# Performance work log

Measured on AMD Instinct MI355X. Metric: run time of the kernel, lower is better.

## Reference

```python
import math
import jax, jax.numpy as jnp
import numpy as np

C_Z = 128
C_HID = 128
B, N = 1, 512


def setup_inputs() -> dict:
    key = jax.random.key(0)
    ks = jax.random.split(key, 8)
    s_in = 1.0 / math.sqrt(C_Z)
    s_hid = 1.0 / math.sqrt(C_HID)
    return {
        "z": jax.random.normal(ks[0], (B, N, N, C_Z), dtype=jnp.float32),
        "residue_mask": jnp.ones((B, N), dtype=jnp.bool_),
        "ln_w": jnp.ones((C_Z,), dtype=jnp.float32),
        "ln_b": jnp.zeros((C_Z,), dtype=jnp.float32),
        "a_w": jax.random.uniform(ks[1], (C_Z, C_HID), jnp.float32, -s_in, s_in),
        "a_b": jax.random.uniform(ks[2], (C_HID,), jnp.float32, -s_in, s_in),
        "b_w": jax.random.uniform(ks[3], (C_Z, C_HID), jnp.float32, -s_in, s_in),
        "b_b": jax.random.uniform(ks[4], (C_HID,), jnp.float32, -s_in, s_in),
        "out_w": jax.random.uniform(ks[5], (C_HID, C_Z), jnp.float32, -s_hid, s_hid),
        "out_b": jax.random.uniform(ks[6], (C_Z,), jnp.float32, -s_hid, s_hid),
    }


def _layernorm(x, w, b, eps=1e-5):
    mu = jnp.mean(x, axis=-1, keepdims=True)
    var = jnp.mean(jnp.square(x - mu), axis=-1, keepdims=True)
    return (x - mu) * jax.lax.rsqrt(var + eps) * w + b


def reference(z, residue_mask, ln_w, ln_b, a_w, a_b, b_w, b_b, out_w, out_b):
    # z: [B, N, N, c_z]
    x = _layernorm(z, ln_w, ln_b)
    a = x @ a_w + a_b  # [B, N, N, c_hid]
    b = x @ b_w + b_b  # [B, N, N, c_hid]
    # outgoing: contract over k -> c_hid independent NxN matmuls
    u = jnp.einsum('bikc,bjkc->bijc', a, b)
    u = (u / math.sqrt(max(z.shape[1], 1))) @ out_w + out_b  # [B, N, N, c_z]
    pair = residue_mask[:, :, None] & residue_mask[:, None, :]  # [B, N, N]
    return u * pair[..., None].astype(u.dtype)
```

## Files before the change

kernel.cpp:

```cpp
#include <hip/hip_runtime.h>

#define NRES 512
#define NN   (NRES * NRES)
#define CZ   128

typedef __attribute__((ext_vector_type(8))) short bf16x8;
typedef __attribute__((ext_vector_type(4))) short s16x4;
typedef __attribute__((ext_vector_type(4))) float f32x4;

static __device__ __forceinline__ short f2bf(float f) {
  union { float f; unsigned u; } v; v.f = f;
  unsigned r = v.u + 0x7fffu + ((v.u >> 16) & 1u);
  return (short)(r >> 16);
}

static __device__ __forceinline__ void gload_lds16(const void* g, void* l) {
  __builtin_amdgcn_global_load_lds(
      (__attribute__((address_space(1))) const void*)g,
      (__attribute__((address_space(3))) void*)l, 16, 0, 0);
}

__global__ __launch_bounds__(256) void k_prep(const float* __restrict__ a_w,
                                              const float* __restrict__ b_w,
                                              const float* __restrict__ out_w,
                                              short* __restrict__ w_cat_t,
                                              short* __restrict__ w_out_t) {
  int idx = blockIdx.x * 256 + threadIdx.x;
  if (idx < 256 * 128) {
    int cc = idx >> 7, zz = idx & 127;
    float v = (cc < 128) ? a_w[zz * 128 + cc] : b_w[zz * 128 + (cc - 128)];
    w_cat_t[idx] = f2bf(v);
  } else if (idx < 256 * 128 + 128 * 128) {
    int i2 = idx - 256 * 128;
    int zz = i2 >> 7, cc = i2 & 127;
    w_out_t[i2] = f2bf(out_w[cc * 128 + zz]);
  }
}

__global__ __launch_bounds__(512, 4) void k_lnproj(const float* __restrict__ z,
                                                   const float* __restrict__ ln_w,
                                                   const float* __restrict__ ln_b,
                                                   const float* __restrict__ a_bias,
                                                   const float* __restrict__ b_bias,
                                                   const short* __restrict__ w_cat_t,
                                                   short* __restrict__ a_t,
                                                   short* __restrict__ b_t) {
  __shared__ short xb[64][136];

  const int tid = threadIdx.x;
  const int bid = (int)blockIdx.x;
  const int sb = ((bid & 7) << 9) | (bid >> 3);
  const int r0 = sb * 64;
  const int row = tid >> 3, seg = tid & 7;

  const float4* zg = (const float4*)(z + (size_t)r0 * CZ);
  float4 v[4];
#pragma unroll
  for (int it = 0; it < 4; ++it) v[it] = zg[row * 32 + seg + it * 8];

  float s = 0.f, s2 = 0.f;
#pragma unroll
  for (int it = 0; it < 4; ++it) {
    s  += v[it].x + v[it].y + v[it].z + v[it].w;
    s2 += v[it].x * v[it].x + v[it].y * v[it].y + v[it].z * v[it].z + v[it].w * v[it].w;
  }
  s  += __shfl_xor(s, 1);  s  += __shfl_xor(s, 2);  s  += __shfl_xor(s, 4);
  s2 += __shfl_xor(s2, 1); s2 += __shfl_xor(s2, 2); s2 += __shfl_xor(s2, 4);
  const float mu = s * (1.f / CZ);
  const float rstd = rsqrtf(s2 * (1.f / CZ) - mu * mu + 1e-5f);

  const float4* lw4 = (const float4*)ln_w;
  const float4* lb4 = (const float4*)ln_b;
#pragma unroll
  for (int it = 0; it < 4; ++it) {
    float4 wv = lw4[seg + it * 8], bv = lb4[seg + it * 8];
    s16x4 pk;
    pk[0] = f2bf((v[it].x - mu) * rstd * wv.x + bv.x);
    pk[1] = f2bf((v[it].y - mu) * rstd * wv.y + bv.y);
    pk[2] = f2bf((v[it].z - mu) * rstd * wv.z + bv.z);
    pk[3] = f2bf((v[it].w - mu) * rstd * wv.w + bv.w);
    *(s16x4*)&xb[row][seg * 4 + it * 32] = pk;
  }
  __syncthreads();

  const int w = tid >> 6, l = tid & 63;
  const int q = l >> 4, n16 = l & 15;
  const f32x4 zf = {0.f, 0.f, 0.f, 0.f};
  f32x4 acc[4][2];
#pragma unroll
  for (int a = 0; a < 4; ++a)
#pragma unroll
    for (int b = 0; b < 2; ++b) acc[a][b] = zf;

#pragma unroll
  for (int kk = 0; kk < 4; ++kk) {
    bf16x8 af[4], bfv[2];
#pragma unroll
    for (int rt = 0; rt < 4; ++rt)
      af[rt] = *(const bf16x8*)&xb[rt * 16 + n16][kk * 32 + q * 8];
#pragma unroll
    for (int ct = 0; ct < 2; ++ct) {
      int col = w * 32 + ct * 16 + n16;
      bfv[ct] = *(const bf16x8*)&w_cat_t[col * 128 + kk * 32 + q * 8];
    }
#pragma unroll
    for (int rt = 0; rt < 4; ++rt)
#pragma unroll
      for (int ct = 0; ct < 2; ++ct)
        acc[rt][ct] = __builtin_amdgcn_mfma_f32_16x16x32_bf16(af[rt], bfv[ct], acc[rt][ct], 0, 0, 0);
  }

  __syncthreads();
  short* tb = &xb[0][0] + w * (16 * 66);
#pragma unroll
  for (int ct = 0; ct < 2; ++ct) {
    const int col = w * 32 + ct * 16 + n16;
    const int ch = col & 127;
    const float bias = (col < 128) ? a_bias[ch] : b_bias[ch];
#pragma unroll
    for (int rt = 0; rt < 4; ++rt) {
      s16x4 pk;
#pragma unroll
      for (int rg = 0; rg < 4; ++rg) pk[rg] = f2bf(acc[rt][ct][rg] + bias);
      *(s16x4*)&tb[n16 * 66 + rt * 16 + q * 4] = pk;
    }
#pragma unroll
    for (int i = 0; i < 2; ++i) {
      int ch_l = i * 8 + (l >> 3);
      int rseg = l & 7;
      bf16x8 t = *(const bf16x8*)&tb[ch_l * 66 + rseg * 8];
      int colg = w * 32 + ct * 16 + ch_l;
      *(bf16x8*)&a_t[(size_t)colg * NN + r0 + rseg * 8] = t;
    }
  }
}

__global__ __launch_bounds__(256, 3) void k_einsum(const short* __restrict__ a_t,
                                                   const short* __restrict__ b_t,
                                                   short* __restrict__ u_bf) {
  __shared__ short smem[128 * 134];
  short* As = smem;
  short* Bs = smem + 128 * 64;

  const int bid = blockIdx.x;
  const int xcd = bid & 7;
  const int g = bid >> 3;
  const int c = (xcd << 4) | (g >> 4);
  const int t = g & 15;
  const int ti = t >> 2, tj = t & 3;

  const short* Ab = a_t + (size_t)c * NN + (size_t)(ti * 128) * NRES;
  const short* Bb = b_t + (size_t)c * NN + (size_t)(tj * 128) * NRES;

  const int tid = threadIdx.x, w = tid >> 6, l = tid & 63;
  const int q = l >> 4, n16 = l & 15;
  const int wr = w >> 1, wc = w & 1;

  const int srow = l >> 3;
  const int schk = l & 7;
  const int gchk = schk ^ srow;

  const f32x4 zf = {0.f, 0.f, 0.f, 0.f};
  f32x4 acc[4][4];
#pragma unroll
  for (int a = 0; a < 4; ++a)
#pragma unroll
    for (int b = 0; b < 4; ++b) acc[a][b] = zf;

  for (int st = 0; st < 8; ++st) {
    const int k0 = st * 64;
    __syncthreads();
#pragma unroll
    for (int i = 0; i < 4; ++i) {
      int r = w * 32 + i * 8 + srow;
      gload_lds16(Ab + (size_t)r * NRES + k0 + gchk * 8, &As[(w * 32 + i * 8) * 64 + l * 8]);
      gload_lds16(Bb + (size_t)r * NRES + k0 + gchk * 8, &Bs[(w * 32 + i * 8) * 64 + l * 8]);
    }
    __syncthreads();

#pragma unroll
    for (int kk = 0; kk < 2; ++kk) {
      bf16x8 af[4], bfv[4];
#pragma unroll
      for (int it = 0; it < 4; ++it) {
        int m = wr * 64 + it * 16 + n16;
        af[it] = *(const bf16x8*)&As[m * 64 + ((kk * 4 + q) ^ (m & 7)) * 8];
      }
#pragma unroll
      for (int jt = 0; jt < 4; ++jt) {
        int n = wc * 64 + jt * 16 + n16;
        bfv[jt] = *(const bf16x8*)&Bs[n * 64 + ((kk * 4 + q) ^ (n & 7)) * 8];
      }
#pragma unroll
      for (int jt = 0; jt < 4; ++jt)
#pragma unroll
        for (int it = 0; it < 4; ++it)
          acc[jt][it] = __builtin_amdgcn_mfma_f32_16x16x32_bf16(bfv[jt], af[it], acc[jt][it], 0, 0, 0);
    }
  }

  __syncthreads();
  const float sc = 0.04419417382415922f;
#pragma unroll
  for (int jt = 0; jt < 4; ++jt)
#pragma unroll
    for (int it = 0; it < 4; ++it) {
      s16x4 pk;
#pragma unroll
      for (int rg = 0; rg < 4; ++rg) pk[rg] = f2bf(acc[jt][it][rg] * sc);
      int il = wr * 64 + it * 16 + n16;
      int jl = wc * 64 + jt * 16 + q * 4;
      *(s16x4*)&smem[il * 134 + jl] = pk;
    }
  __syncthreads();

  short* ub = u_bf + (size_t)c * NN + (size_t)(ti * 128) * NRES + tj * 128;
#pragma unroll
  for (int vv = 0; vv < 8; ++vv) {
    int CH = vv * 256 + tid;
    int i = CH >> 4, js = CH & 15;
    bf16x8 tv = *(const bf16x8*)&smem[i * 134 + js * 8];
    *(bf16x8*)&ub[(size_t)i * NRES + js * 8] = tv;
  }
}

#define US_S 130
__global__ __launch_bounds__(256, 3) void k_outproj(const short* __restrict__ u_bf,
                                                    const short* __restrict__ w_out_t,
                                                    const float* __restrict__ out_b,
                                                    const int* __restrict__ mask,
                                                    float* __restrict__ out) {
  __shared__ short Us[128 * US_S];

  const int bid = (int)blockIdx.x;
  const int sb = ((bid & 7) << 8) | (bid >> 3);
  const int m0 = sb * 128;
  const int tid = threadIdx.x, w = tid >> 6, l = tid & 63;
  const int q = l >> 4, n16 = l & 15;
  const int wz = w >> 1, wm = w & 1;

  {
    const int mseg = tid & 15;
    const int cb = tid >> 4;
#pragma unroll
    for (int it = 0; it < 8; ++it) {
      int cc = it * 16 + cb;
      bf16x8 vv = *(const bf16x8*)(u_bf + (size_t)cc * NN + m0 + mseg * 8);
      int base = cc * US_S + mseg * 8;
#pragma unroll
      for (int wi = 0; wi < 4; ++wi) {
        int pk = ((int)(unsigned short)vv[2 * wi + 1] << 16) | (unsigned short)vv[2 * wi];
        *(int*)&Us[base + 2 * wi] = pk;
      }
    }
  }
  __syncthreads();

  const f32x4 zf = {0.f, 0.f, 0.f, 0.f};
  f32x4 acc[4][4];
#pragma unroll
  for (int a = 0; a < 4; ++a)
#pragma unroll
    for (int b = 0; b < 4; ++b) acc[a][b] = zf;

#pragma unroll
  for (int kk = 0; kk < 4; ++kk) {
    bf16x8 af[4];
#pragma unroll
    for (int rt = 0; rt < 4; ++rt) {
      int zz = wz * 64 + rt * 16 + n16;
      af[rt] = *(const bf16x8*)&w_out_t[zz * 128 + kk * 32 + q * 8];
    }
    bf16x8 bfv[4];
#pragma unroll
    for (int ct = 0; ct < 4; ++ct) {
      int mm = wm * 64 + ct * 16 + n16;
      int c0 = kk * 32 + q * 8;
      bf16x8 tv;
#pragma unroll
      for (int j = 0; j < 8; ++j) tv[j] = Us[(c0 + j) * US_S + mm];
      bfv[ct] = tv;
    }
#pragma unroll
    for (int rt = 0; rt < 4; ++rt)
#pragma unroll
      for (int ct = 0; ct < 4; ++ct)
        acc[rt][ct] = __builtin_amdgcn_mfma_f32_16x16x32_bf16(af[rt], bfv[ct], acc[rt][ct], 0, 0, 0);
  }

  const int i_blk = m0 >> 9;
  const int j0 = m0 & 511;
  const int mi = mask[i_blk];
#pragma unroll
  for (int ct = 0; ct < 4; ++ct) {
    int mm = wm * 64 + ct * 16 + n16;
    int on = (mi != 0) && (mask[j0 + mm] != 0);
#pragma unroll
    for (int rt = 0; rt < 4; ++rt) {
      int z0 = wz * 64 + rt * 16 + q * 4;
      float4 bias = *(const float4*)&out_b[z0];
      float4 r;
      r.x = on ? acc[rt][ct][0] + bias.x : 0.f;
      r.y = on ? acc[rt][ct][1] + bias.y : 0.f;
      r.z = on ? acc[rt][ct][2] + bias.z : 0.f;
      r.w = on ? acc[rt][ct][3] + bias.w : 0.f;
      *(float4*)&out[(size_t)(m0 + mm) * CZ + z0] = r;
    }
  }
}

extern "C" void kernel_launch(void* const* d_in, const int* in_sizes, int n_in,
                              void* d_out, int out_size, void* d_ws, size_t ws_size,
                              hipStream_t stream) {
  const float* z     = (const float*)d_in[0];
  const int*   mask  = (const int*)d_in[1];
  const float* ln_w  = (const float*)d_in[2];
  const float* ln_b  = (const float*)d_in[3];
  const float* a_w   = (const float*)d_in[4];
  const float* a_b   = (const float*)d_in[5];
  const float* b_w   = (const float*)d_in[6];
  const float* b_b   = (const float*)d_in[7];
  const float* out_w = (const float*)d_in[8];
  const float* out_b = (const float*)d_in[9];
  float* out = (float*)d_out;

  char* p = (char*)d_ws;
  short* w_cat_t = (short*)p; p += (size_t)256 * 128 * 2;
  short* w_out_t = (short*)p; p += (size_t)128 * 128 * 2;
  short* a_t  = (short*)p; p += (size_t)NN * 128 * 2;
  short* b_t  = (short*)p; p += (size_t)NN * 128 * 2;
  short* u_bf = (short*)p; p += (size_t)NN * 128 * 2;

  hipLaunchKernelGGL(k_prep,    dim3(192),  dim3(256), 0, stream, a_w, b_w, out_w, w_cat_t, w_out_t);
  hipLaunchKernelGGL(k_lnproj,  dim3(4096), dim3(512), 0, stream, z, ln_w, ln_b, a_b, b_b, w_cat_t, a_t, b_t);
  hipLaunchKernelGGL(k_einsum,  dim3(2048), dim3(256), 0, stream, a_t, b_t, u_bf);
  hipLaunchKernelGGL(k_outproj, dim3(2048), dim3(256), 0, stream, u_bf, w_out_t, out_b, mask, out);
}
```

Measured before the change: 387.5 us.

## Process 128 rows per LN-projection block to widen transposed output stores

Each k_lnproj block now handles two 64-row sub-tiles. It keeps the bf16 projection results in registers, then stages them through a larger LDS buffer so every channel writes 128 contiguous rows (256 bytes) into the transposed a_t/b_t layout instead of 64. The grid halves and the XCD-swizzled block ordering is dropped. The aim is to make the scattered transposed writes more coalesced, at the cost of a much larger LDS footprint (about 50 KB), which may reduce occupancy below the launch_bounds target, plus extra barriers.

```diff
diff --git a/kernel.cpp b/kernel.cpp
--- a/kernel.cpp
+++ b/kernel.cpp
@@ -46,92 +46,115 @@
                                                    short* __restrict__ a_t,
                                                    short* __restrict__ b_t) {
   __shared__ short xb[64][136];
+  __shared__ short stage[128 * 130];
 
   const int tid = threadIdx.x;
-  const int bid = (int)blockIdx.x;
-  const int sb = ((bid & 7) << 9) | (bid >> 3);
-  const int r0 = sb * 64;
-  const int row = tid >> 3, seg = tid & 7;
-
-  const float4* zg = (const float4*)(z + (size_t)r0 * CZ);
-  float4 v[4];
-#pragma unroll
-  for (int it = 0; it < 4; ++it) v[it] = zg[row * 32 + seg + it * 8];
-
-  float s = 0.f, s2 = 0.f;
-#pragma unroll
-  for (int it = 0; it < 4; ++it) {
-    s  += v[it].x + v[it].y + v[it].z + v[it].w;
-    s2 += v[it].x * v[it].x + v[it].y * v[it].y + v[it].z * v[it].z + v[it].w * v[it].w;
-  }
-  s  += __shfl_xor(s, 1);  s  += __shfl_xor(s, 2);  s  += __shfl_xor(s, 4);
-  s2 += __shfl_xor(s2, 1); s2 += __shfl_xor(s2, 2); s2 += __shfl_xor(s2, 4);
-  const float mu = s * (1.f / CZ);
-  const float rstd = rsqrtf(s2 * (1.f / CZ) - mu * mu + 1e-5f);
-
-  const float4* lw4 = (const float4*)ln_w;
-  const float4* lb4 = (const float4*)ln_b;
-#pragma unroll
-  for (int it = 0; it < 4; ++it) {
-    float4 wv = lw4[seg + it * 8], bv = lb4[seg + it * 8];
-    s16x4 pk;
-    pk[0] = f2bf((v[it].x - mu) * rstd * wv.x + bv.x);
-    pk[1] = f2bf((v[it].y - mu) * rstd * wv.y + bv.y);
-    pk[2] = f2bf((v[it].z - mu) * rstd * wv.z + bv.z);
-    pk[3] = f2bf((v[it].w - mu) * rstd * wv.w + bv.w);
-    *(s16x4*)&xb[row][seg * 4 + it * 32] = pk;
-  }
-  __syncthreads();
-
+  const int r0 = (int)blockIdx.x * 128;
+  const int row = tid >> 3, seg8 = tid & 7;
   const int w = tid >> 6, l = tid & 63;
   const int q = l >> 4, n16 = l & 15;
-  const f32x4 zf = {0.f, 0.f, 0.f, 0.f};
-  f32x4 acc[4][2];
-#pragma unroll
-  for (int a = 0; a < 4; ++a)
-#pragma unroll
-    for (int b = 0; b < 2; ++b) acc[a][b] = zf;
-
-#pragma unroll
-  for (int kk = 0; kk < 4; ++kk) {
-    bf16x8 af[4], bfv[2];
-#pragma unroll
-    for (int rt = 0; rt < 4; ++rt)
-      af[rt] = *(const bf16x8*)&xb[rt * 16 + n16][kk * 32 + q * 8];
+
+  s16x4 park[2][2][4];
+
+#pragma unroll
+  for (int sub = 0; sub < 2; ++sub) {
+    const int rs = r0 + sub * 64;
+
+    const float4* zg = (const float4*)(z + (size_t)rs * CZ);
+    float4 v[4];
+#pragma unroll
+    for (int it = 0; it < 4; ++it) v[it] = zg[row * 32 + seg8 + it * 8];
+
+    float s = 0.f, s2 = 0.f;
+#pragma unroll
+    for (int it = 0; it < 4; ++it) {
+      s  += v[it].x + v[it].y + v[it].z + v[it].w;
+      s2 += v[it].x * v[it].x + v[it].y * v[it].y + v[it].z * v[it].z + v[it].w * v[it].w;
+    }
+    s  += __shfl_xor(s, 1);  s  += __shfl_xor(s, 2);  s  += __shfl_xor(s, 4);
+    s2 += __shfl_xor(s2, 1); s2 += __shfl_xor(s2, 2); s2 += __shfl_xor(s2, 4);
+    const float mu = s * (1.f / CZ);
+    const float rstd = rsqrtf(s2 * (1.f / CZ) - mu * mu + 1e-5f);
+
+    const float4* lw4 = (const float4*)ln_w;
+    const float4* lb4 = (const float4*)ln_b;
+#pragma unroll
+    for (int it = 0; it < 4; ++it) {
+      float4 wv = lw4[seg8 + it * 8], bv = lb4[seg8 + it * 8];
+      s16x4 pk;
+      pk[0] = f2bf((v[it].x - mu) * rstd * wv.x + bv.x);
+      pk[1] = f2bf((v[it].y - mu) * rstd * wv.y + bv.y);
+      pk[2] = f2bf((v[it].z - mu) * rstd * wv.z + bv.z);
+      pk[3] = f2bf((v[it].w - mu) * rstd * wv.w + bv.w);
+      *(s16x4*)&xb[row][seg8 * 4 + it * 32] = pk;
+    }
+    __syncthreads();
+
+    f32x4 acc[4][2];
+    const f32x4 zf = {0.f, 0.f, 0.f, 0.f};
+#pragma unroll
+    for (int a = 0; a < 4; ++a)
+#pragma unroll
+      for (int b = 0; b < 2; ++b) acc[a][b] = zf;
+
+#pragma unroll
+    for (int kk = 0; kk < 4; ++kk) {
+      bf16x8 af[4], bfv[2];
+#pragma unroll
+      for (int rt = 0; rt < 4; ++rt)
+        af[rt] = *(const bf16x8*)&xb[rt * 16 + n16][kk * 32 + q * 8];
+#pragma unroll
+      for (int ct = 0; ct < 2; ++ct) {
+        int col = w * 32 + ct * 16 + n16;
+        bfv[ct] = *(const bf16x8*)&w_cat_t[col * 128 + kk * 32 + q * 8];
+      }
+#pragma unroll
+      for (int rt = 0; rt < 4; ++rt)
+#pragma unroll
+        for (int ct = 0; ct < 2; ++ct)
+          acc[rt][ct] = __builtin_amdgcn_mfma_f32_16x16x32_bf16(af[rt], bfv[ct], acc[rt][ct], 0, 0, 0);
+    }
+
 #pragma unroll
     for (int ct = 0; ct < 2; ++ct) {
-      int col = w * 32 + ct * 16 + n16;
-      bfv[ct] = *(const bf16x8*)&w_cat_t[col * 128 + kk * 32 + q * 8];
-    }
-#pragma unroll
-    for (int rt = 0; rt < 4; ++rt)
-#pragma unroll
-      for (int ct = 0; ct < 2; ++ct)
-        acc[rt][ct] = __builtin_amdgcn_mfma_f32_16x16x32_bf16(af[rt], bfv[ct], acc[rt][ct], 0, 0, 0);
-  }
-
-  __syncthreads();
-  short* tb = &xb[0][0] + w * (16 * 66);
-#pragma unroll
-  for (int ct = 0; ct < 2; ++ct) {
-    const int col = w * 32 + ct * 16 + n16;
-    const int ch = col & 127;
-    const float bias = (col < 128) ? a_bias[ch] : b_bias[ch];
-#pragma unroll
-    for (int rt = 0; rt < 4; ++rt) {
-      s16x4 pk;
-#pragma unroll
-      for (int rg = 0; rg < 4; ++rg) pk[rg] = f2bf(acc[rt][ct][rg] + bias);
-      *(s16x4*)&tb[n16 * 66 + rt * 16 + q * 4] = pk;
-    }
-#pragma unroll
-    for (int i = 0; i < 2; ++i) {
-      int ch_l = i * 8 + (l >> 3);
-      int rseg = l & 7;
-      bf16x8 t = *(const bf16x8*)&tb[ch_l * 66 + rseg * 8];
-      int colg = w * 32 + ct * 16 + ch_l;
-      *(bf16x8*)&a_t[(size_t)colg * NN + r0 + rseg * 8] = t;
-    }
+      const int col = w * 32 + ct * 16 + n16;
+      const int ch = col & 127;
+      const float bias = (col < 128) ? a_bias[ch] : b_bias[ch];
+#pragma unroll
+      for (int rt = 0; rt < 4; ++rt) {
+        s16x4 pk;
+#pragma unroll
+        for (int rg = 0; rg < 4; ++rg) pk[rg] = f2bf(acc[rt][ct][rg] + bias);
+        park[sub][ct][rt] = pk;
+      }
+    }
+    __syncthreads();
+  }
+
+  const int seg = tid & 15, cq = tid >> 4;
+#pragma unroll
+  for (int g = 0; g < 2; ++g) {
+    if ((w >> 2) == g) {
+#pragma unroll
+      for (int sub = 0; sub < 2; ++sub)
+#pragma unroll
+        for (int ct = 0; ct < 2; ++ct)
+#pragma unroll
+          for (int rt = 0; rt < 4; ++rt) {
+            int ch_local = (w & 3) * 32 + ct * 16 + n16;
+            int row_local = sub * 64 + rt * 16 + q * 4;
+            *(s16x4*)&stage[ch_local * 130 + row_local] = park[sub][ct][rt];
+          }
+    }
+    __syncthreads();
+#pragma unroll
+    for (int it = 0; it < 4; ++it) {
+      int ch_l = it * 32 + cq;
+      bf16x8 t = *(const bf16x8*)&stage[ch_l * 130 + seg * 8];
+      int ch_global = g * 128 + ch_l;
+      *(bf16x8*)&a_t[(size_t)ch_global * NN + r0 + seg * 8] = t;
+    }
+    __syncthreads();
   }
 }
 
@@ -332,7 +355,7 @@
   short* u_bf = (short*)p; p += (size_t)NN * 128 * 2;
 
   hipLaunchKernelGGL(k_prep,    dim3(192),  dim3(256), 0, stream, a_w, b_w, out_w, w_cat_t, w_out_t);
-  hipLaunchKernelGGL(k_lnproj,  dim3(4096), dim3(512), 0, stream, z, ln_w, ln_b, a_b, b_b, w_cat_t, a_t, b_t);
+  hipLaunchKernelGGL(k_lnproj,  dim3(2048), dim3(512), 0, stream, z, ln_w, ln_b, a_b, b_b, w_cat_t, a_t, b_t);
   hipLaunchKernelGGL(k_einsum,  dim3(2048), dim3(256), 0, stream, a_t, b_t, u_bf);
   hipLaunchKernelGGL(k_outproj, dim3(2048), dim3(256), 0, stream, u_bf, w_out_t, out_b, mask, out);
 }
```

New measurement: 374.4 us. 1.04x faster.
